# Performance work log

Hardware: AMD Instinct MI355X
Metric: run time of the kernel (lower is better)

Reference implementation:

```python
import jax, jax.numpy as jnp
import numpy as np

B, SMAX, TMAX, D = 8, 4096, 4096, 528


def setup_inputs() -> dict:
    key = jax.random.key(0)
    ks = jax.random.split(key, 20)
    src_lens = (np.arange(B) * 256 + 2048).astype(np.int64)  # 2048..3840, sum 23552
    tgt_lens = (np.arange(B) * 224 + 2304).astype(np.int64)  # 2304..3872, sum 24704
    Ns, Nt = int(src_lens.sum()), int(tgt_lens.sum())
    N = Ns + Nt  # 48256 packed coarse points (src then tgt)
    src_mask = jnp.asarray(np.arange(SMAX)[None, :] < src_lens[:, None])
    tgt_mask = jnp.asarray(np.arange(TMAX)[None, :] < tgt_lens[:, None])
    sics = np.concatenate([b * SMAX + np.arange(l) for b, l in enumerate(src_lens)])
    tics = np.concatenate([b * TMAX + np.arange(l) for b, l in enumerate(tgt_lens)])
    w = lambda k, shape: (jax.random.normal(k, shape, jnp.float32) * 0.02)
    return dict(
        geo_feats=jax.random.normal(ks[0], (N, D), jnp.float32),
        pcd=jax.random.normal(ks[1], (N, 3), jnp.float32),
        Wi1=w(ks[2], (528, 528)), bi1=w(ks[3], (528,)),
        Wi2=w(ks[4], (1024, 528)), bi2=w(ks[5], (1024,)),
        Wc1=w(ks[6], (528, 528)), bc1=w(ks[7], (528,)),
        Wc2=w(ks[8], (1024, 528)), bc2=w(ks[9], (1024,)),
        Ws1=w(ks[10], (512, 2576)), bs1=w(ks[11], (512,)),
        Ws2=w(ks[12], (256, 512)), bs2=w(ks[13], (256,)),
        Ws3=w(ks[14], (1, 256)), bs3=w(ks[15], (1,)),
        src_mask=src_mask, tgt_mask=tgt_mask,
        src_ind_coarse_split=jnp.asarray(sics, jnp.int32),
        tgt_ind_coarse_split=jnp.asarray(tics, jnp.int32),
        src_ind_coarse=jnp.arange(Ns, dtype=jnp.int32),
        tgt_ind_coarse=Ns + jnp.arange(Nt, dtype=jnp.int32),
    )


def _scatter(vals, flat_idx, b, n, d):
    # split_feats: zeros[b*n, d]; out[flat_idx] = vals; view(b, n, d)
    return jnp.zeros((b * n, d), vals.dtype).at[flat_idx].set(vals).reshape(b, n, d)


def _pw(x, W, b):
    # pointwise Conv1d(in->out, k=1) as a batched matmul over positions
    return jnp.einsum('bnd,od->bno', x, W) + b


def reference(geo_feats, pcd, Wi1, bi1, Wi2, bi2, Wc1, bc1, Wc2, bc2,
              Ws1, bs1, Ws2, bs2, Ws3, bs3,
              src_mask, tgt_mask, src_ind_coarse_split, tgt_ind_coarse_split,
              src_ind_coarse, tgt_ind_coarse):
    b, smax = src_mask.shape
    tmax = tgt_mask.shape[1]
    d = geo_feats.shape[-1]

    # split_feats: ragged gather -> padded [B, pts_max, D]
    src_feats = _scatter(geo_feats[src_ind_coarse], src_ind_coarse_split, b, smax, d)
    tgt_feats = _scatter(geo_feats[tgt_ind_coarse], tgt_ind_coarse_split, b, tmax, d)
    s_pcd = _scatter(pcd[src_ind_coarse], src_ind_coarse_split, b, smax, 3)
    t_pcd = _scatter(pcd[tgt_ind_coarse], tgt_ind_coarse_split, b, tmax, 3)

    sm = src_mask.astype(src_feats.dtype)
    tm = tgt_mask.astype(tgt_feats.dtype)

    # inst_global over valid src points (per-sample slice -> masked mean)
    h = jax.nn.relu(_pw(src_feats, Wi1, bi1))
    h = jax.nn.relu(_pw(h, Wi2, bi2))                      # [B, Smax, 1024]
    inst_g = jnp.einsum('bno,bn->bo', h, sm) / sm.sum(1, keepdims=True)

    # category_global over valid tgt points
    g = jax.nn.relu(_pw(tgt_feats, Wc1, bc1))
    g = jax.nn.relu(_pw(g, Wc2, bc2))                      # [B, Tmax, 1024]
    cat_g = jnp.einsum('bno,bn->bo', g, tm) / tm.sum(1, keepdims=True)

    # scale_net on concat(src_feats, inst_g, cat_g) without materializing [B,N,2576]:
    # split first conv weight over the concat axis; globals contribute per-batch constants
    Ws1_s, Ws1_i, Ws1_c = Ws1[:, :d], Ws1[:, d:d + 1024], Ws1[:, d + 1024:]
    glob = inst_g @ Ws1_i.T + cat_g @ Ws1_c.T + bs1        # [B, 512]
    z = jax.nn.relu(jnp.einsum('bnd,od->bno', src_feats, Ws1_s) + glob[:, None, :])
    z = jax.nn.relu(_pw(z, Ws2, bs2))                      # [B, Smax, 256]
    s = _pw(z, Ws3, bs3)                                   # [B, Smax, 1]
    scale_mat = jax.nn.sigmoid(s).transpose(0, 2, 1) - 0.5  # [B, 1, Smax]

    inv = 1.0 / jnp.sqrt(jnp.asarray(d, src_feats.dtype))
    return (src_feats * inv, tgt_feats * inv, s_pcd, t_pcd, scale_mat)
```

## Files before the change

kernel.cpp:

```cpp
#include <hip/hip_runtime.h>
#include <hip/hip_bf16.h>
#include <cstdint>
#include <cstddef>

typedef float f32x4 __attribute__((ext_vector_type(4)));
typedef __bf16 bf16x8v __attribute__((ext_vector_type(8)));
typedef __hip_bfloat16 bf16;

__device__ __forceinline__ void gld16(const void* g, void* l) {
  __builtin_amdgcn_global_load_lds((const __attribute__((address_space(1))) void*)g,
                                   (__attribute__((address_space(3))) void*)l, 16, 0, 0);
}

__device__ __forceinline__ int xcd_swz(int orig, int nwg) {
  int q = nwg >> 3, r = nwg & 7;
  int x = orig & 7, i = orig >> 3;
  return (x < r ? x * (q + 1) : r * (q + 1) + (x - r) * q) + i;
}


struct PrepP {
  const float* Wsrc[6];
  bf16* Wdst[6];
  int sld[6], rows[6], K[6], Kpad[6];
  int off[10];
  float* zbuf; int ztotal;
  const float* geo; bf16* geo_b; int Nrows;
  const int* sics; const int* tics; int Ns, Nt; int* cnt;
};

__global__ void prep_kernel(PrepP P) {
  int blk = blockIdx.x;
  int job = 0;
  while (job < 8 && blk >= P.off[job + 1]) ++job;
  int local = blk - P.off[job];
  if (job < 6) {
    int i = local * 256 + threadIdx.x;
    int kp = P.Kpad[job];
    int total = P.rows[job] * kp;
    if (i < total) {
      int r = i / kp, k = i - r * kp;
      float v = (k < P.K[job]) ? P.Wsrc[job][(size_t)r * P.sld[job] + k] : 0.f;
      P.Wdst[job][i] = __float2bfloat16(v);
    }
  } else if (job == 6) {
    int i = local * 256 + threadIdx.x;
    if (i < P.ztotal) P.zbuf[i] = 0.f;
  } else if (job == 7) {
    int t = local * 256 + threadIdx.x;
    int row = t / 72, c8 = t - row * 72;
    if (row < P.Nrows) {
      int col = c8 * 8;
      bf16* dst = P.geo_b + (size_t)row * 576 + col;
      if (c8 < 66) {
        const float* s = P.geo + (size_t)row * 528 + col;
        float4 f0 = ((const float4*)s)[0], f1 = ((const float4*)s)[1];
        bf16 h[8] = {__float2bfloat16(f0.x), __float2bfloat16(f0.y),
                     __float2bfloat16(f0.z), __float2bfloat16(f0.w),
                     __float2bfloat16(f1.x), __float2bfloat16(f1.y),
                     __float2bfloat16(f1.z), __float2bfloat16(f1.w)};
        ((uint4*)dst)[0] = *(uint4*)h;
      } else {
        uint4 z = {0u, 0u, 0u, 0u};
        ((uint4*)dst)[0] = z;
      }
    }
  } else {
    int j = local * 256 + threadIdx.x;
    if (j < P.Ns) {
      if (j == 0) { P.cnt[0] = 0; P.cnt[8] = P.Ns; }
      else { int b = P.sics[j] >> 12; if ((P.sics[j - 1] >> 12) != b) P.cnt[b] = j; }
    }
    if (j < P.Nt) {
      if (j == 0) { P.cnt[9] = 0; P.cnt[17] = P.Nt; }
      else { int b = P.tics[j] >> 12; if ((P.tics[j - 1] >> 12) != b) P.cnt[9 + b] = j; }
    }
  }
}

__device__ __forceinline__ void gemm_core(
    const bf16* __restrict__ Aptr, int lda,
    const bf16* __restrict__ Bw, int ldb,
    int m0, int n0, int kiters,
    bf16* __restrict__ lA, bf16* __restrict__ lB,
    f32x4 acc[4][4])
{
  const int tid  = threadIdx.x;
  const int lane = tid & 63;
  const int quad = lane >> 4;
  const int l16  = lane & 15;
  const int wr   = tid >> 7;
  const int wc   = (tid >> 6) & 1;
  const int srow = tid >> 2;
  const int scol = (tid & 3) << 3;
  const bf16* aA0 = Aptr + (size_t)(m0 + srow) * lda + scol;
  const bf16* aA1 = aA0 + (size_t)64 * lda;
  const bf16* aB0 = Bw + (size_t)(n0 + srow) * ldb + scol;
  const bf16* aB1 = aB0 + (size_t)64 * ldb;
  bf16* lA00 = lA + tid * 8;        bf16* lA01 = lA + 2048 + tid * 8;
  bf16* lA10 = lA + 4096 + tid * 8; bf16* lA11 = lA + 6144 + tid * 8;
  bf16* lB00 = lB + tid * 8;        bf16* lB01 = lB + 2048 + tid * 8;
  bf16* lB10 = lB + 4096 + tid * 8; bf16* lB11 = lB + 6144 + tid * 8;

  for (int k = 0; k < kiters; ++k) {
    const int k0 = k * 64;
    gld16(aA0 + k0, lA00);      gld16(aA1 + k0, lA01);
    gld16(aA0 + k0 + 32, lA10); gld16(aA1 + k0 + 32, lA11);
    gld16(aB0 + k0, lB00);      gld16(aB1 + k0, lB01);
    gld16(aB0 + k0 + 32, lB10); gld16(aB1 + k0 + 32, lB11);
    __syncthreads();
#pragma unroll
    for (int kk = 0; kk < 2; ++kk) {
      bf16x8v af[4], bfr[4];
#pragma unroll
      for (int i = 0; i < 4; ++i) {
        af[i]  = *(const bf16x8v*)&lA[kk * 4096 + (wr * 64 + i * 16 + l16) * 32 + quad * 8];
        bfr[i] = *(const bf16x8v*)&lB[kk * 4096 + (wc * 64 + i * 16 + l16) * 32 + quad * 8];
      }
#pragma unroll
      for (int mi = 0; mi < 4; ++mi)
#pragma unroll
        for (int ni = 0; ni < 4; ++ni)
          acc[mi][ni] = __builtin_amdgcn_mfma_f32_16x16x32_bf16(af[mi], bfr[ni], acc[mi][ni], 0, 0, 0);
    }
    __syncthreads();
  }
}

__global__ __launch_bounds__(256, 2)
void kernelA(const bf16* __restrict__ geo_b,
             const bf16* __restrict__ Wi1b, const bf16* __restrict__ Wc1b,
             const bf16* __restrict__ Ws1sb,
             const float* __restrict__ bi1, const float* __restrict__ bc1,
             bf16* __restrict__ big_s, bf16* __restrict__ big_t,
             bf16* __restrict__ zpre, int Ms, int Mt)
{
  __shared__ alignas(16) bf16 lA[8192], lB[8192];
  const int x = xcd_swz(blockIdx.x, gridDim.x);
  const int e0 = Ms * 5, e1 = e0 + Mt * 5;
  const bf16 *A, *B; const float* bias = nullptr; bf16* out;
  int m0, n0, ldo, epi;
  if (x < e0) {
    int mt = x / 5, nt = x - mt * 5;
    m0 = mt * 128; n0 = nt * 128;
    A = geo_b; B = Wi1b; bias = bi1; out = big_s; ldo = 576; epi = 0;
  } else if (x < e1) {
    int y = x - e0; int mt = y / 5, nt = y - mt * 5;
    m0 = mt * 128; n0 = nt * 128;
    A = geo_b + (size_t)Ms * 128 * 576; B = Wc1b; bias = bc1; out = big_t; ldo = 576; epi = 0;
  } else {
    int y = x - e1; int mt = y / 4, nt = y - mt * 4;
    m0 = mt * 128; n0 = nt * 128;
    A = geo_b; B = Ws1sb; out = zpre; ldo = 512; epi = 1;
  }

  f32x4 acc[4][4];
  const f32x4 z4 = {0.f, 0.f, 0.f, 0.f};
#pragma unroll
  for (int i = 0; i < 4; ++i)
#pragma unroll
    for (int j = 0; j < 4; ++j) acc[i][j] = z4;

  gemm_core(A, 576, B, 576, m0, n0, 9, lA, lB, acc);

  const int lane = threadIdx.x & 63, quad = lane >> 4, l16 = lane & 15;
  const int wr = threadIdx.x >> 7, wc = (threadIdx.x >> 6) & 1;
#pragma unroll
  for (int mi = 0; mi < 4; ++mi) {
#pragma unroll
    for (int r = 0; r < 4; ++r) {
      const int row = m0 + wr * 64 + mi * 16 + quad * 4 + r;
#pragma unroll
      for (int ni = 0; ni < 4; ++ni) {
        const int col = n0 + wc * 64 + ni * 16 + l16;
        if (epi == 0) {
          if (col < 528)
            out[(size_t)row * ldo + col] = __float2bfloat16(fmaxf(acc[mi][ni][r] + bias[col], 0.f));
          else if (col < 576)
            out[(size_t)row * ldo + col] = __float2bfloat16(0.f);
        } else {
          out[(size_t)row * ldo + col] = __float2bfloat16(acc[mi][ni][r]);
        }
      }
    }
  }
}

__global__ __launch_bounds__(256, 2)
void kernelB(const bf16* __restrict__ big_s, const bf16* __restrict__ big_t,
             const bf16* __restrict__ Wi2b, const bf16* __restrict__ Wc2b,
             const float* __restrict__ bi2, const float* __restrict__ bc2,
             float* __restrict__ iacc, float* __restrict__ cacc,
             const int* __restrict__ sics, const int* __restrict__ tics,
             int Ms, int Mt,
             const float* __restrict__ geo, const float* __restrict__ pcd,
             const int* __restrict__ cnt,
             float* __restrict__ out0, float* __restrict__ out1,
             float* __restrict__ out2, float* __restrict__ out3,
             int Ns, float inv)
{
  __shared__ alignas(16) bf16 lA[8192], lB[8192];
  const int xb = blockIdx.x;
  const int e0 = Ms * 8, e1 = e0 + Mt * 8;
  if (xb >= e1) {
    int f = xb - e1;
    int lane = threadIdx.x & 63;
    int rv = f * 4 + (threadIdx.x >> 6);
    bool is_t = rv >= 32768;
    int pos = is_t ? rv - 32768 : rv;
    int b = pos >> 12, r = pos & 4095;
    int base = is_t ? cnt[9 + b] : cnt[b];
    int lim  = (is_t ? cnt[9 + b + 1] : cnt[b + 1]) - base;
    float* op = (is_t ? out1 : out0) + (size_t)pos * 528;
    float* pp = (is_t ? out3 : out2) + (size_t)pos * 3;
    if (r < lim) {
      int sr = (is_t ? Ns : 0) + base + r;
      const float4* g = (const float4*)(geo + (size_t)sr * 528);
      for (int d = lane; d < 132; d += 64) {
        float4 v = g[d];
        float4 s = {v.x * inv, v.y * inv, v.z * inv, v.w * inv};
        ((float4*)op)[d] = s;
      }
      if (lane < 3) pp[lane] = pcd[(size_t)sr * 3 + lane];
    } else {
      float4 z = {0.f, 0.f, 0.f, 0.f};
      for (int d = lane; d < 132; d += 64) ((float4*)op)[d] = z;
      if (lane < 3) pp[lane] = 0.f;
    }
    return;
  }
  const int x = xcd_swz(xb, e1);
  const bf16 *A, *B; const float* bias; float* red; const int* ridx;
  int m0, n0;
  if (x < e0) {
    int mt = x / 8, nt = x - mt * 8;
    m0 = mt * 128; n0 = nt * 128;
    A = big_s; B = Wi2b; bias = bi2; red = iacc; ridx = sics;
  } else {
    int y = x - e0; int mt = y / 8, nt = y - mt * 8;
    m0 = mt * 128; n0 = nt * 128;
    A = big_t; B = Wc2b; bias = bc2; red = cacc; ridx = tics;
  }

  f32x4 acc[4][4];
  const f32x4 z4 = {0.f, 0.f, 0.f, 0.f};
#pragma unroll
  for (int i = 0; i < 4; ++i)
#pragma unroll
    for (int j = 0; j < 4; ++j) acc[i][j] = z4;

  gemm_core(A, 576, B, 576, m0, n0, 9, lA, lB, acc);

  const int lane = threadIdx.x & 63, quad = lane >> 4, l16 = lane & 15;
  const int wr = threadIdx.x >> 7, wc = (threadIdx.x >> 6) & 1;
  const int b0r = ridx[m0] >> 12;
#pragma unroll
  for (int ni = 0; ni < 4; ++ni) {
    const int col = n0 + wc * 64 + ni * 16 + l16;
    const float bcol = bias[col];
#pragma unroll
    for (int mi = 0; mi < 4; ++mi) {
      float v0 = 0.f, v1 = 0.f;
#pragma unroll
      for (int r = 0; r < 4; ++r) {
        const int row = m0 + wr * 64 + mi * 16 + quad * 4 + r;
        const float v = fmaxf(acc[mi][ni][r] + bcol, 0.f);
        const int b = ridx[row] >> 12;
        if (b == b0r) v0 += v; else v1 += v;
      }
      v0 += __shfl_xor(v0, 16, 64); v0 += __shfl_xor(v0, 32, 64);
      v1 += __shfl_xor(v1, 16, 64); v1 += __shfl_xor(v1, 32, 64);
      if (quad == 0) {
        atomicAdd(&red[b0r * 1024 + col], v0);
        if (b0r + 1 < 8 && v1 != 0.f) atomicAdd(&red[(b0r + 1) * 1024 + col], v1);
      }
    }
  }
}

__global__ __launch_bounds__(256, 2)
void kernelC(const bf16* __restrict__ zpre, const bf16* __restrict__ Ws2b,
             const float* __restrict__ bs2, const float* __restrict__ Ws3,
             const float* __restrict__ globv, const int* __restrict__ sics,
             float* __restrict__ sbuf)
{
  __shared__ alignas(16) bf16 lA[8192], lB[8192];
  const int x = xcd_swz(blockIdx.x, gridDim.x);
  const int m0 = (x >> 1) * 128, n0 = (x & 1) * 128;
  const int tid  = threadIdx.x;
  const int lane = tid & 63, quad = lane >> 4, l16 = lane & 15;
  const int wr = tid >> 7, wc = (tid >> 6) & 1;
  const int srow = tid >> 2;
  const int scol = (tid & 3) << 3;

  const int r0g = m0 + srow, r1g = r0g + 64;
  const float* gv0 = globv + ((size_t)(sics[r0g] >> 12) << 9);
  const float* gv1 = globv + ((size_t)(sics[r1g] >> 12) << 9);
  const bf16* za0 = zpre + (size_t)r0g * 512 + scol;
  const bf16* za1 = zpre + (size_t)r1g * 512 + scol;
  const bf16* aB0 = Ws2b + (size_t)(n0 + srow) * 512 + scol;
  const bf16* aB1 = aB0 + (size_t)64 * 512;
  bf16* lB00 = lB + tid * 8;        bf16* lB01 = lB + 2048 + tid * 8;
  bf16* lB10 = lB + 4096 + tid * 8; bf16* lB11 = lB + 6144 + tid * 8;

  f32x4 acc[4][4];
  const f32x4 z4 = {0.f, 0.f, 0.f, 0.f};
#pragma unroll
  for (int i = 0; i < 4; ++i)
#pragma unroll
    for (int j = 0; j < 4; ++j) acc[i][j] = z4;

  auto stageA = [&](const bf16* src, const float* gv, int col, bf16* dst) {
    uint4 u = *(const uint4*)src;
    bf16 e[8]; *(uint4*)e = u;
    bf16 o[8];
#pragma unroll
    for (int i = 0; i < 8; ++i)
      o[i] = __float2bfloat16(fmaxf(__bfloat162float(e[i]) + gv[col + i], 0.f));
    *(uint4*)dst = *(uint4*)o;
  };

  for (int k = 0; k < 8; ++k) {
    const int k0 = k * 64;
    gld16(aB0 + k0, lB00);      gld16(aB1 + k0, lB01);
    gld16(aB0 + k0 + 32, lB10); gld16(aB1 + k0 + 32, lB11);
    stageA(za0 + k0,      gv0, k0 + scol,      lA + tid * 8);
    stageA(za1 + k0,      gv1, k0 + scol,      lA + 2048 + tid * 8);
    stageA(za0 + k0 + 32, gv0, k0 + scol + 32, lA + 4096 + tid * 8);
    stageA(za1 + k0 + 32, gv1, k0 + scol + 32, lA + 6144 + tid * 8);
    __syncthreads();
#pragma unroll
    for (int kk = 0; kk < 2; ++kk) {
      bf16x8v af[4], bfr[4];
#pragma unroll
      for (int i = 0; i < 4; ++i) {
        af[i]  = *(const bf16x8v*)&lA[kk * 4096 + (wr * 64 + i * 16 + l16) * 32 + quad * 8];
        bfr[i] = *(const bf16x8v*)&lB[kk * 4096 + (wc * 64 + i * 16 + l16) * 32 + quad * 8];
      }
#pragma unroll
      for (int mi = 0; mi < 4; ++mi)
#pragma unroll
        for (int ni = 0; ni < 4; ++ni)
          acc[mi][ni] = __builtin_amdgcn_mfma_f32_16x16x32_bf16(af[mi], bfr[ni], acc[mi][ni], 0, 0, 0);
    }
    __syncthreads();
  }

#pragma unroll
  for (int mi = 0; mi < 4; ++mi) {
#pragma unroll
    for (int r = 0; r < 4; ++r) {
      const int row = m0 + wr * 64 + mi * 16 + quad * 4 + r;
      float p = 0.f;
#pragma unroll
      for (int ni = 0; ni < 4; ++ni) {
        const int col = n0 + wc * 64 + ni * 16 + l16;
        p += fmaxf(acc[mi][ni][r] + bs2[col], 0.f) * Ws3[col];
      }
      p += __shfl_xor(p, 1, 64); p += __shfl_xor(p, 2, 64);
      p += __shfl_xor(p, 4, 64); p += __shfl_xor(p, 8, 64);
      if (l16 == 0) atomicAdd(&sbuf[row], p);
    }
  }
}

__global__ __launch_bounds__(256) void glob_kernel(const float* __restrict__ iacc,
                                                   const float* __restrict__ cacc,
                                                   const int* __restrict__ cnt,
                                                   const float* __restrict__ Ws1,
                                                   const float* __restrict__ bs1,
                                                   float* __restrict__ globv) {
  int w    = (blockIdx.x * 256 + threadIdx.x) >> 6;
  int lane = threadIdx.x & 63;
  int b = w >> 9;
  int o = w & 511;
  const float* wi  = Ws1 + (size_t)o * 2576 + 528;
  const float* wcp = Ws1 + (size_t)o * 2576 + 1552;
  float a1 = 0.f, a2 = 0.f;
  for (int k = lane; k < 1024; k += 64) {
    a1 += iacc[b * 1024 + k] * wi[k];
    a2 += cacc[b * 1024 + k] * wcp[k];
  }
  for (int off = 32; off; off >>= 1) {
    a1 += __shfl_xor(a1, off, 64);
    a2 += __shfl_xor(a2, off, 64);
  }
  if (lane == 0) {
    float ns = (float)(cnt[b + 1] - cnt[b]);
    float nt = (float)(cnt[9 + b + 1] - cnt[9 + b]);
    globv[b * 512 + o] = bs1[o] + a1 / ns + a2 / nt;
  }
}

__global__ __launch_bounds__(256) void s_empty_kernel(const float* __restrict__ globv,
                                                      const float* __restrict__ Ws2,
                                                      const float* __restrict__ bs2,
                                                      const float* __restrict__ Ws3,
                                                      const float* __restrict__ bs3,
                                                      float* __restrict__ semp) {
  __shared__ float zrow[512];
  __shared__ float wsum[4];
  int b = blockIdx.x, t = threadIdx.x;
  zrow[t]       = fmaxf(globv[b * 512 + t], 0.f);
  zrow[t + 256] = fmaxf(globv[b * 512 + t + 256], 0.f);
  __syncthreads();
  int w = t >> 6, lane = t & 63;
  float ws = 0.f;
  for (int tt = w * 64; tt < w * 64 + 64; ++tt) {
    float a = 0.f;
#pragma unroll
    for (int oi = 0; oi < 8; ++oi) {
      int o = lane + oi * 64;
      a += zrow[o] * Ws2[(size_t)tt * 512 + o];
    }
    for (int off = 32; off; off >>= 1) a += __shfl_xor(a, off, 64);
    if (lane == 0) ws += fmaxf(a + bs2[tt], 0.f) * Ws3[tt];
  }
  if (lane == 0) wsum[w] = ws;
  __syncthreads();
  if (t == 0) semp[b] = wsum[0] + wsum[1] + wsum[2] + wsum[3] + bs3[0];
}

__global__ void scale_kernel(const float* __restrict__ sbuf,
                             const float* __restrict__ semp,
                             const int* __restrict__ cnt,
                             const float* __restrict__ bs3,
                             float* __restrict__ out4) {
  int i = blockIdx.x * 256 + threadIdx.x;
  if (i >= 32768) return;
  int b = i >> 12, r = i & 4095;
  int base = cnt[b];
  int lim = cnt[b + 1] - base;
  float s = (r < lim) ? sbuf[base + r] + bs3[0] : semp[b];
  out4[i] = 1.f / (1.f + expf(-s)) - 0.5f;
}


extern "C" void kernel_launch(void* const* d_in, const int* in_sizes, int n_in,
                              void* d_out, int out_size, void* d_ws, size_t ws_size,
                              hipStream_t stream) {
  const float* geo = (const float*)d_in[0];
  const float* pcd = (const float*)d_in[1];
  const float* Wi1 = (const float*)d_in[2];
  const float* bi1 = (const float*)d_in[3];
  const float* Wi2 = (const float*)d_in[4];
  const float* bi2 = (const float*)d_in[5];
  const float* Wc1 = (const float*)d_in[6];
  const float* bc1 = (const float*)d_in[7];
  const float* Wc2 = (const float*)d_in[8];
  const float* bc2 = (const float*)d_in[9];
  const float* Ws1 = (const float*)d_in[10];
  const float* bs1 = (const float*)d_in[11];
  const float* Ws2 = (const float*)d_in[12];
  const float* bs2 = (const float*)d_in[13];
  const float* Ws3 = (const float*)d_in[14];
  const float* bs3 = (const float*)d_in[15];
  const int* sics = (const int*)d_in[18];
  const int* tics = (const int*)d_in[19];
  const int Ns = in_sizes[18];
  const int Nt = in_sizes[19];
  const int Ms = Ns / 128, Mt = Nt / 128;
  const int Nrows = Ns + Nt;

  float* out0 = (float*)d_out;
  float* out1 = out0 + (size_t)8 * 4096 * 528;
  float* out2 = out1 + (size_t)8 * 4096 * 528;
  float* out3 = out2 + (size_t)8 * 4096 * 3;
  float* out4 = out3 + (size_t)8 * 4096 * 3;

  char* wp = (char*)d_ws;
  auto alloc = [&](size_t bytes) -> void* {
    void* p = (void*)wp;
    wp += (bytes + 255) & ~(size_t)255;
    return p;
  };
  int*   cnt   = (int*)  alloc(128);
  float* iacc  = (float*)alloc((size_t)8 * 1024 * 4);
  float* cacc  = (float*)alloc((size_t)8 * 1024 * 4);
  float* sbuf  = (float*)alloc((size_t)Ns * 4);
  float* globb = (float*)alloc((size_t)8 * 512 * 4);
  float* semp  = (float*)alloc(64);
  bf16* Wi1b  = (bf16*)alloc((size_t)640  * 576 * 2);
  bf16* Wi2b  = (bf16*)alloc((size_t)1024 * 576 * 2);
  bf16* Wc1b  = (bf16*)alloc((size_t)640  * 576 * 2);
  bf16* Wc2b  = (bf16*)alloc((size_t)1024 * 576 * 2);
  bf16* Ws1sb = (bf16*)alloc((size_t)512  * 576 * 2);
  bf16* Ws2b  = (bf16*)alloc((size_t)256  * 512 * 2);
  bf16* geo_b = (bf16*)alloc((size_t)Nrows * 576 * 2);
  bf16* big_s = (bf16*)alloc((size_t)Ns * 576 * 2);
  bf16* big_t = (bf16*)alloc((size_t)Nt * 576 * 2);
  bf16* zpre  = (bf16*)alloc((size_t)Ns * 512 * 2);

  float inv = 1.0f / sqrtf(528.0f);

  PrepP P;
  {
    const float* srcs[6] = {Wi1, Wi2, Wc1, Wc2, Ws1, Ws2};
    bf16* dsts[6]        = {Wi1b, Wi2b, Wc1b, Wc2b, Ws1sb, Ws2b};
    int slds[6] = {528, 528, 528, 528, 2576, 512};
    int rows[6] = {528, 1024, 528, 1024, 512, 256};
    int Ks[6]   = {528, 528, 528, 528, 528, 512};
    int Kps[6]  = {576, 576, 576, 576, 576, 512};
    int nblk = 0;
    for (int i = 0; i < 6; ++i) {
      P.Wsrc[i] = srcs[i]; P.Wdst[i] = dsts[i]; P.sld[i] = slds[i];
      P.rows[i] = rows[i]; P.K[i] = Ks[i]; P.Kpad[i] = Kps[i];
      P.off[i] = nblk;
      nblk += (rows[i] * Kps[i] + 255) / 256;
    }
    P.off[6] = nblk;
    P.zbuf = iacc; P.ztotal = 8192 + 8192 + Ns;
    nblk += (P.ztotal + 255) / 256;
    P.off[7] = nblk;
    P.geo = geo; P.geo_b = geo_b; P.Nrows = Nrows;
    nblk += ((Nrows * 72) + 255) / 256;
    P.off[8] = nblk;
    P.sics = sics; P.tics = tics; P.Ns = Ns; P.Nt = Nt; P.cnt = cnt;
    int n = Ns > Nt ? Ns : Nt;
    nblk += (n + 255) / 256;
    P.off[9] = nblk;
    prep_kernel<<<dim3(nblk), dim3(256), 0, stream>>>(P);
  }

  kernelA<<<dim3(Ms * 5 + Mt * 5 + Ms * 4), dim3(256), 0, stream>>>(
      geo_b, Wi1b, Wc1b, Ws1sb, bi1, bc1, big_s, big_t, zpre, Ms, Mt);

  kernelB<<<dim3(Ms * 8 + Mt * 8 + 16384), dim3(256), 0, stream>>>(
      big_s, big_t, Wi2b, Wc2b, bi2, bc2, iacc, cacc, sics, tics, Ms, Mt,
      geo, pcd, cnt, out0, out1, out2, out3, Ns, inv);

  glob_kernel<<<dim3(1024), dim3(256), 0, stream>>>(iacc, cacc, cnt, Ws1, bs1, globb);
  s_empty_kernel<<<dim3(8), dim3(256), 0, stream>>>(globb, Ws2, bs2, Ws3, bs3, semp);
  kernelC<<<dim3(Ms * 2), dim3(256), 0, stream>>>(zpre, Ws2b, bs2, Ws3, globb, sics, sbuf);
  scale_kernel<<<dim3(128), dim3(256), 0, stream>>>(sbuf, semp, cnt, bs3, out4);
}
```

Measured before the change: 536.5 us.

## Fuse fp32-to-bf16 geo conversion into kernelA loads and drop XCD swizzle

Removes the prep pass that converted geo_feats to a padded bf16 copy. kernelA now reads fp32 rows directly, converts them in registers and stores them to LDS, while B tiles still use async global-to-LDS loads. This saves a full write and re-read of the bf16 copy, but each source tile is now converted in several blocks (5 or 9 per row tile) and the fp32 A reads are synchronous. The XCD-aware block index swizzle is also removed from kernelA, kernelB and kernelC, which may change L2 locality.

```diff
diff --git a/kernel.cpp b/kernel.cpp
--- a/kernel.cpp
+++ b/kernel.cpp
@@ -12,27 +12,20 @@
                                    (__attribute__((address_space(3))) void*)l, 16, 0, 0);
 }
 
-__device__ __forceinline__ int xcd_swz(int orig, int nwg) {
-  int q = nwg >> 3, r = nwg & 7;
-  int x = orig & 7, i = orig >> 3;
-  return (x < r ? x * (q + 1) : r * (q + 1) + (x - r) * q) + i;
-}
-
 
 struct PrepP {
   const float* Wsrc[6];
   bf16* Wdst[6];
   int sld[6], rows[6], K[6], Kpad[6];
-  int off[10];
+  int off[9];
   float* zbuf; int ztotal;
-  const float* geo; bf16* geo_b; int Nrows;
   const int* sics; const int* tics; int Ns, Nt; int* cnt;
 };
 
 __global__ void prep_kernel(PrepP P) {
   int blk = blockIdx.x;
   int job = 0;
-  while (job < 8 && blk >= P.off[job + 1]) ++job;
+  while (job < 7 && blk >= P.off[job + 1]) ++job;
   int local = blk - P.off[job];
   if (job < 6) {
     int i = local * 256 + threadIdx.x;
@@ -46,25 +39,6 @@
   } else if (job == 6) {
     int i = local * 256 + threadIdx.x;
     if (i < P.ztotal) P.zbuf[i] = 0.f;
-  } else if (job == 7) {
-    int t = local * 256 + threadIdx.x;
-    int row = t / 72, c8 = t - row * 72;
-    if (row < P.Nrows) {
-      int col = c8 * 8;
-      bf16* dst = P.geo_b + (size_t)row * 576 + col;
-      if (c8 < 66) {
-        const float* s = P.geo + (size_t)row * 528 + col;
-        float4 f0 = ((const float4*)s)[0], f1 = ((const float4*)s)[1];
-        bf16 h[8] = {__float2bfloat16(f0.x), __float2bfloat16(f0.y),
-                     __float2bfloat16(f0.z), __float2bfloat16(f0.w),
-                     __float2bfloat16(f1.x), __float2bfloat16(f1.y),
-                     __float2bfloat16(f1.z), __float2bfloat16(f1.w)};
-        ((uint4*)dst)[0] = *(uint4*)h;
-      } else {
-        uint4 z = {0u, 0u, 0u, 0u};
-        ((uint4*)dst)[0] = z;
-      }
-    }
   } else {
     int j = local * 256 + threadIdx.x;
     if (j < P.Ns) {
@@ -128,31 +102,43 @@
 }
 
 __global__ __launch_bounds__(256, 2)
-void kernelA(const bf16* __restrict__ geo_b,
+void kernelA(const float* __restrict__ geo,
              const bf16* __restrict__ Wi1b, const bf16* __restrict__ Wc1b,
              const bf16* __restrict__ Ws1sb,
              const float* __restrict__ bi1, const float* __restrict__ bc1,
              bf16* __restrict__ big_s, bf16* __restrict__ big_t,
-             bf16* __restrict__ zpre, int Ms, int Mt)
+             bf16* __restrict__ zpre, int Ms, int Mt, int Ns)
 {
   __shared__ alignas(16) bf16 lA[8192], lB[8192];
-  const int x = xcd_swz(blockIdx.x, gridDim.x);
+  const int x = blockIdx.x;
   const int e0 = Ms * 5, e1 = e0 + Mt * 5;
-  const bf16 *A, *B; const float* bias = nullptr; bf16* out;
+  const float* Ag; const bf16* B; const float* bias = nullptr; bf16* out;
   int m0, n0, ldo, epi;
   if (x < e0) {
     int mt = x / 5, nt = x - mt * 5;
     m0 = mt * 128; n0 = nt * 128;
-    A = geo_b; B = Wi1b; bias = bi1; out = big_s; ldo = 576; epi = 0;
+    Ag = geo; B = Wi1b; bias = bi1; out = big_s; ldo = 576; epi = 0;
   } else if (x < e1) {
     int y = x - e0; int mt = y / 5, nt = y - mt * 5;
     m0 = mt * 128; n0 = nt * 128;
-    A = geo_b + (size_t)Ms * 128 * 576; B = Wc1b; bias = bc1; out = big_t; ldo = 576; epi = 0;
+    Ag = geo + (size_t)Ns * 528; B = Wc1b; bias = bc1; out = big_t; ldo = 576; epi = 0;
   } else {
     int y = x - e1; int mt = y / 4, nt = y - mt * 4;
     m0 = mt * 128; n0 = nt * 128;
-    A = geo_b; B = Ws1sb; out = zpre; ldo = 512; epi = 1;
-  }
+    Ag = geo; B = Ws1sb; out = zpre; ldo = 512; epi = 1;
+  }
+
+  const int tid  = threadIdx.x;
+  const int lane = tid & 63, quad = lane >> 4, l16 = lane & 15;
+  const int wr = tid >> 7, wc = (tid >> 6) & 1;
+  const int srow = tid >> 2;
+  const int scol = (tid & 3) << 3;
+  const float* gA0 = Ag + (size_t)(m0 + srow) * 528;
+  const float* gA1 = gA0 + (size_t)64 * 528;
+  const bf16* aB0 = B + (size_t)(n0 + srow) * 576 + scol;
+  const bf16* aB1 = aB0 + (size_t)64 * 576;
+  bf16* lB00 = lB + tid * 8;        bf16* lB01 = lB + 2048 + tid * 8;
+  bf16* lB10 = lB + 4096 + tid * 8; bf16* lB11 = lB + 6144 + tid * 8;
 
   f32x4 acc[4][4];
   const f32x4 z4 = {0.f, 0.f, 0.f, 0.f};
@@ -161,10 +147,48 @@
 #pragma unroll
     for (int j = 0; j < 4; ++j) acc[i][j] = z4;
 
-  gemm_core(A, 576, B, 576, m0, n0, 9, lA, lB, acc);
-
-  const int lane = threadIdx.x & 63, quad = lane >> 4, l16 = lane & 15;
-  const int wr = threadIdx.x >> 7, wc = (threadIdx.x >> 6) & 1;
+  auto cvt8 = [&](const float* rowp, int col, bf16* dst) {
+    bf16 o[8];
+    if (col < 528) {
+      const float* s = rowp + col;
+      float4 f0 = ((const float4*)s)[0], f1 = ((const float4*)s)[1];
+      o[0] = __float2bfloat16(f0.x); o[1] = __float2bfloat16(f0.y);
+      o[2] = __float2bfloat16(f0.z); o[3] = __float2bfloat16(f0.w);
+      o[4] = __float2bfloat16(f1.x); o[5] = __float2bfloat16(f1.y);
+      o[6] = __float2bfloat16(f1.z); o[7] = __float2bfloat16(f1.w);
+    } else {
+#pragma unroll
+      for (int i = 0; i < 8; ++i) o[i] = __float2bfloat16(0.f);
+    }
+    *(uint4*)dst = *(uint4*)o;
+  };
+
+  for (int k = 0; k < 9; ++k) {
+    const int k0 = k * 64;
+    gld16(aB0 + k0, lB00);      gld16(aB1 + k0, lB01);
+    gld16(aB0 + k0 + 32, lB10); gld16(aB1 + k0 + 32, lB11);
+    cvt8(gA0, k0 + scol,      lA + tid * 8);
+    cvt8(gA1, k0 + scol,      lA + 2048 + tid * 8);
+    cvt8(gA0, k0 + scol + 32, lA + 4096 + tid * 8);
+    cvt8(gA1, k0 + scol + 32, lA + 6144 + tid * 8);
+    __syncthreads();
+#pragma unroll
+    for (int kk = 0; kk < 2; ++kk) {
+      bf16x8v af[4], bfr[4];
+#pragma unroll
+      for (int i = 0; i < 4; ++i) {
+        af[i]  = *(const bf16x8v*)&lA[kk * 4096 + (wr * 64 + i * 16 + l16) * 32 + quad * 8];
+        bfr[i] = *(const bf16x8v*)&lB[kk * 4096 + (wc * 64 + i * 16 + l16) * 32 + quad * 8];
+      }
+#pragma unroll
+      for (int mi = 0; mi < 4; ++mi)
+#pragma unroll
+        for (int ni = 0; ni < 4; ++ni)
+          acc[mi][ni] = __builtin_amdgcn_mfma_f32_16x16x32_bf16(af[mi], bfr[ni], acc[mi][ni], 0, 0, 0);
+    }
+    __syncthreads();
+  }
+
 #pragma unroll
   for (int mi = 0; mi < 4; ++mi) {
 #pragma unroll
@@ -200,10 +224,10 @@
              int Ns, float inv)
 {
   __shared__ alignas(16) bf16 lA[8192], lB[8192];
-  const int xb = blockIdx.x;
+  const int x = blockIdx.x;
   const int e0 = Ms * 8, e1 = e0 + Mt * 8;
-  if (xb >= e1) {
-    int f = xb - e1;
+  if (x >= e1) {
+    int f = x - e1;
     int lane = threadIdx.x & 63;
     int rv = f * 4 + (threadIdx.x >> 6);
     bool is_t = rv >= 32768;
@@ -229,7 +253,6 @@
     }
     return;
   }
-  const int x = xcd_swz(xb, e1);
   const bf16 *A, *B; const float* bias; float* red; const int* ridx;
   int m0, n0;
   if (x < e0) {
@@ -285,7 +308,7 @@
              float* __restrict__ sbuf)
 {
   __shared__ alignas(16) bf16 lA[8192], lB[8192];
-  const int x = xcd_swz(blockIdx.x, gridDim.x);
+  const int x = blockIdx.x;
   const int m0 = (x >> 1) * 128, n0 = (x & 1) * 128;
   const int tid  = threadIdx.x;
   const int lane = tid & 63, quad = lane >> 4, l16 = lane & 15;
@@ -460,7 +483,6 @@
   const int Ns = in_sizes[18];
   const int Nt = in_sizes[19];
   const int Ms = Ns / 128, Mt = Nt / 128;
-  const int Nrows = Ns + Nt;
 
   float* out0 = (float*)d_out;
   float* out1 = out0 + (size_t)8 * 4096 * 528;
@@ -486,7 +508,6 @@
   bf16* Wc2b  = (bf16*)alloc((size_t)1024 * 576 * 2);
   bf16* Ws1sb = (bf16*)alloc((size_t)512  * 576 * 2);
   bf16* Ws2b  = (bf16*)alloc((size_t)256  * 512 * 2);
-  bf16* geo_b = (bf16*)alloc((size_t)Nrows * 576 * 2);
   bf16* big_s = (bf16*)alloc((size_t)Ns * 576 * 2);
   bf16* big_t = (bf16*)alloc((size_t)Nt * 576 * 2);
   bf16* zpre  = (bf16*)alloc((size_t)Ns * 512 * 2);
@@ -512,18 +533,15 @@
     P.zbuf = iacc; P.ztotal = 8192 + 8192 + Ns;
     nblk += (P.ztotal + 255) / 256;
     P.off[7] = nblk;
-    P.geo = geo; P.geo_b = geo_b; P.Nrows = Nrows;
-    nblk += ((Nrows * 72) + 255) / 256;
-    P.off[8] = nblk;
     P.sics = sics; P.tics = tics; P.Ns = Ns; P.Nt = Nt; P.cnt = cnt;
     int n = Ns > Nt ? Ns : Nt;
     nblk += (n + 255) / 256;
-    P.off[9] = nblk;
+    P.off[8] = nblk;
     prep_kernel<<<dim3(nblk), dim3(256), 0, stream>>>(P);
   }
 
   kernelA<<<dim3(Ms * 5 + Mt * 5 + Ms * 4), dim3(256), 0, stream>>>(
-      geo_b, Wi1b, Wc1b, Ws1sb, bi1, bc1, big_s, big_t, zpre, Ms, Mt);
+      geo, Wi1b, Wc1b, Ws1sb, bi1, bc1, big_s, big_t, zpre, Ms, Mt, Ns);
 
   kernelB<<<dim3(Ms * 8 + Mt * 8 + 16384), dim3(256), 0, stream>>>(
       big_s, big_t, Wi2b, Wc2b, bi2, bc2, iacc, cacc, sics, tics, Ms, Mt,
```

Measured after the change: 567.9 us. +5.9%, slower.
